# Performance work log

Measured on AMD Instinct MI355X. Metric: run time of the kernel, lower is better.

The kernel has to match this reference:

```python
import jax, jax.numpy as jnp
import numpy as np

N_DRUG, N_DIS, E, D = 10000, 15000, 1048576, 128

def setup_inputs() -> dict:
    key = jax.random.key(0)
    k = jax.random.split(key, 6)
    return {
        "z_drug": jax.random.normal(k[0], (N_DRUG, D), dtype=jnp.float32),
        "z_disease": jax.random.normal(k[1], (N_DIS, D), dtype=jnp.float32),
        "row": jax.random.randint(k[2], (E,), 0, N_DRUG),
        "col": jax.random.randint(k[3], (E,), 0, N_DIS),
        "W1": jax.random.normal(k[4], (2 * D, D), dtype=jnp.float32) * (1.0 / np.sqrt(2 * D)),
        "b1": jnp.zeros((D,), dtype=jnp.float32),
        "W2": jax.random.normal(k[5], (D, 1), dtype=jnp.float32) * (1.0 / np.sqrt(D)),
        "b2": jnp.zeros((1,), dtype=jnp.float32),
    }

def reference(z_drug, z_disease, row, col, W1, b1, W2, b2):
    # gather per-edge embeddings and concatenate: [E, 2D]
    z = jnp.concatenate([z_drug[row], z_disease[col]], axis=-1)
    h = jax.nn.relu(z @ W1 + b1)          # [E, D]
    out = h @ W2 + b2                      # [E, 1]
    return out.reshape(-1)                 # [E]
```

## Files before the change

kernel.cpp:

```cpp
#include <hip/hip_runtime.h>

typedef __attribute__((ext_vector_type(8))) short short8;
typedef __attribute__((ext_vector_type(4))) float floatx4;
typedef _Float16 half8 __attribute__((ext_vector_type(8)));
typedef _Float16 half4 __attribute__((ext_vector_type(4)));
typedef _Float16 half2v __attribute__((ext_vector_type(2)));

static __device__ __forceinline__ unsigned short f2bf(float x) {
    unsigned int u = __builtin_bit_cast(unsigned int, x);
    unsigned int r = (u + 0x7FFFu + ((u >> 16) & 1u)) >> 16;
    return (unsigned short)r;
}

__global__ void prep_w1(const float* __restrict__ W1, unsigned short* __restrict__ w1t) {
    int i = blockIdx.x * 256 + threadIdx.x;
    int n = i >> 8;
    int k = i & 255;
    w1t[n * 256 + k] = f2bf(W1[k * 128 + n]);
}

__global__ __launch_bounds__(256, 2) void factor_gemm(
    const float* __restrict__ zd, const float* __restrict__ zs,
    const unsigned short* __restrict__ w1t, const float* __restrict__ b1,
    _Float16* __restrict__ ud, _Float16* __restrict__ us,
    int ndrows, int nsrows, int ntd)
{
    const int tid  = threadIdx.x;
    const int lane = tid & 63;
    const int wave = tid >> 6;
    const int wh   = wave >> 1;
    const int we   = wave & 1;
    const int l15  = lane & 15;
    const int quad = lane >> 4;

    const int b = blockIdx.x;
    const bool isD = (b < ntd);
    const float* __restrict__ z = isD ? zd : zs;
    _Float16* __restrict__ u = isD ? ud : us;
    const int nrows = isD ? ndrows : nsrows;
    const int m0    = (isD ? b : b - ntd) * 64;
    const int koff0 = isD ? 0 : 128;

    short8 wfrag[16];
    #pragma unroll
    for (int s = 0; s < 4; ++s)
        #pragma unroll
        for (int mt = 0; mt < 4; ++mt)
            wfrag[s * 4 + mt] = *reinterpret_cast<const short8*>(
                &w1t[(size_t)(wh * 64 + mt * 16 + l15) * 256 + koff0 + s * 32 + quad * 8]);

    floatx4 acc[2][4];
    #pragma unroll
    for (int mt = 0; mt < 4; ++mt) {
        floatx4 bb = *reinterpret_cast<const floatx4*>(&b1[wh * 64 + mt * 16 + quad * 4]);
        bb *= 0.5f;
        acc[0][mt] = bb;
        acc[1][mt] = bb;
    }

    int rowi[2], rowc[2];
    #pragma unroll
    for (int et = 0; et < 2; ++et) {
        rowi[et] = m0 + we * 32 + et * 16 + l15;
        rowc[et] = rowi[et] < nrows ? rowi[et] : nrows - 1;
    }

    #pragma unroll
    for (int s = 0; s < 4; ++s) {
        short8 bf[2];
        #pragma unroll
        for (int et = 0; et < 2; ++et) {
            const float* src = &z[(size_t)rowc[et] * 128 + s * 32 + quad * 8];
            floatx4 lo = *reinterpret_cast<const floatx4*>(src);
            floatx4 hi = *reinterpret_cast<const floatx4*>(src + 4);
            short8 t;
            t[0] = (short)f2bf(lo[0]); t[1] = (short)f2bf(lo[1]);
            t[2] = (short)f2bf(lo[2]); t[3] = (short)f2bf(lo[3]);
            t[4] = (short)f2bf(hi[0]); t[5] = (short)f2bf(hi[1]);
            t[6] = (short)f2bf(hi[2]); t[7] = (short)f2bf(hi[3]);
            bf[et] = t;
        }
        #pragma unroll
        for (int et = 0; et < 2; ++et)
            #pragma unroll
            for (int mt = 0; mt < 4; ++mt)
                acc[et][mt] = __builtin_amdgcn_mfma_f32_16x16x32_bf16(
                    wfrag[s * 4 + mt], bf[et], acc[et][mt], 0, 0, 0);
    }

    #pragma unroll
    for (int et = 0; et < 2; ++et) {
        if (rowi[et] < nrows) {
            #pragma unroll
            for (int mt = 0; mt < 4; ++mt) {
                half4 hv;
                #pragma unroll
                for (int rr = 0; rr < 4; ++rr) hv[rr] = (_Float16)acc[et][mt][rr];
                *reinterpret_cast<half4*>(
                    &u[(size_t)rowi[et] * 128 + wh * 64 + mt * 16 + quad * 4]) = hv;
            }
        }
    }
}

__global__ __launch_bounds__(256, 4) void edge_eval(
    const _Float16* __restrict__ ud, const _Float16* __restrict__ us,
    const int* __restrict__ row, const int* __restrict__ col,
    const float* __restrict__ w2, const float* __restrict__ b2,
    float* __restrict__ out, int nchunks)
{
    const int tid  = threadIdx.x;
    const int lane = tid & 63;
    const int wave = tid >> 6;
    const int le   = lane >> 3;
    const int q    = lane & 7;
    const int lslot = wave * 8 + le;

#if __has_builtin(__builtin_amdgcn_fdot2)
    half2v w2h[8];
    #pragma unroll
    for (int i = 0; i < 2; ++i)
        #pragma unroll
        for (int p = 0; p < 4; ++p) {
            half2v t;
            t[0] = (_Float16)w2[i * 64 + q * 8 + 2 * p];
            t[1] = (_Float16)w2[i * 64 + q * 8 + 2 * p + 1];
            w2h[i * 4 + p] = t;
        }
#else
    float w2r[16];
    #pragma unroll
    for (int i = 0; i < 2; ++i) {
        *reinterpret_cast<floatx4*>(&w2r[i * 8]) =
            *reinterpret_cast<const floatx4*>(&w2[i * 64 + q * 8]);
        *reinterpret_cast<floatx4*>(&w2r[i * 8 + 4]) =
            *reinterpret_cast<const floatx4*>(&w2[i * 64 + q * 8 + 4]);
    }
#endif
    const float b2v = b2[0];
    const int G = gridDim.x;
    const int b = blockIdx.x;
    const int NC = nchunks / G;

    int ridx[4], cidx[4];
    half8 Ur[4][2], Vr[4][2];

#define LIDX(slot, j)                                                          \
    if ((j) < NC) {                                                            \
        int e = (b + (j) * G) * 32 + lslot;                                    \
        ridx[slot] = row[e]; cidx[slot] = col[e];                              \
    }

#define GATH(slot, j)                                                          \
    if ((j) < NC) {                                                            \
        const _Float16* up = ud + (size_t)ridx[slot] * 128 + q * 8;            \
        const _Float16* vp = us + (size_t)cidx[slot] * 128 + q * 8;            \
        Ur[slot][0] = *reinterpret_cast<const half8*>(up);                     \
        Ur[slot][1] = *reinterpret_cast<const half8*>(up + 64);                \
        Vr[slot][0] = *reinterpret_cast<const half8*>(vp);                     \
        Vr[slot][1] = *reinterpret_cast<const half8*>(vp + 64);                \
    }

#if __has_builtin(__builtin_amdgcn_fdot2)
#define DOT(slot, accv)                                                        \
    _Pragma("unroll")                                                          \
    for (int i = 0; i < 2; ++i) {                                              \
        half8 s8 = Ur[slot][i] + Vr[slot][i];                                  \
        s8 = __builtin_elementwise_max(s8, (half8)(_Float16)0.f);              \
        _Pragma("unroll")                                                      \
        for (int p = 0; p < 4; ++p) {                                          \
            half2v pr; pr[0] = s8[2 * p]; pr[1] = s8[2 * p + 1];               \
            accv = __builtin_amdgcn_fdot2(pr, w2h[i * 4 + p], accv, false);    \
        }                                                                      \
    }
#else
#define DOT(slot, accv)                                                        \
    _Pragma("unroll")                                                          \
    for (int i = 0; i < 2; ++i) {                                              \
        half8 s8 = Ur[slot][i] + Vr[slot][i];                                  \
        s8 = __builtin_elementwise_max(s8, (half8)(_Float16)0.f);              \
        _Pragma("unroll")                                                      \
        for (int j2 = 0; j2 < 8; ++j2)                                         \
            accv += (float)s8[j2] * w2r[i * 8 + j2];                           \
    }
#endif

#define COMP(slot, j)                                                          \
    if ((j) < NC) {                                                            \
        float acc = 0.f;                                                       \
        DOT(slot, acc)                                                         \
        acc += __shfl_xor(acc, 1);                                             \
        acc += __shfl_xor(acc, 2);                                             \
        acc += __shfl_xor(acc, 4);                                             \
        if (q == 0) out[(b + (j) * G) * 32 + lslot] = acc + b2v;               \
    }

    LIDX(0, 0) LIDX(1, 1) LIDX(2, 2)
    GATH(0, 0) GATH(1, 1) GATH(2, 2)
    LIDX(3, 3) LIDX(0, 4)

    for (int jb = 0; jb < NC; jb += 4) {
        GATH(3, jb + 3) LIDX(1, jb + 5) COMP(0, jb)
        GATH(0, jb + 4) LIDX(2, jb + 6) COMP(1, jb + 1)
        GATH(1, jb + 5) LIDX(3, jb + 7) COMP(2, jb + 2)
        GATH(2, jb + 6) LIDX(0, jb + 8) COMP(3, jb + 3)
    }
#undef LIDX
#undef GATH
#undef DOT
#undef COMP
}

extern "C" void kernel_launch(void* const* d_in, const int* in_sizes, int n_in,
                              void* d_out, int out_size, void* d_ws, size_t ws_size,
                              hipStream_t stream) {
    const float* zd = (const float*)d_in[0];
    const float* zs = (const float*)d_in[1];
    const int*   row = (const int*)d_in[2];
    const int*   col = (const int*)d_in[3];
    const float* W1 = (const float*)d_in[4];
    const float* b1 = (const float*)d_in[5];
    const float* w2 = (const float*)d_in[6];
    const float* b2 = (const float*)d_in[7];
    float* out = (float*)d_out;

    const int nd = in_sizes[0];
    const int ns = in_sizes[1];
    const int E  = in_sizes[2];
    const int ndrows = nd / 128;
    const int nsrows = ns / 128;

    unsigned short* w1t = (unsigned short*)d_ws;
    _Float16* ud = (_Float16*)((char*)d_ws + 128 * 256 * sizeof(unsigned short));
    _Float16* us = ud + (size_t)ndrows * 128;

    hipLaunchKernelGGL(prep_w1, dim3(128), dim3(256), 0, stream, W1, w1t);

    const int ntd = (ndrows + 63) / 64;
    const int nts = (nsrows + 63) / 64;
    hipLaunchKernelGGL(factor_gemm, dim3(ntd + nts), dim3(256), 0, stream,
                       zd, zs, w1t, b1, ud, us, ndrows, nsrows, ntd);

    const int nchunks = E / 32;
    const int egrid = 1024;
    hipLaunchKernelGGL(edge_eval, dim3(egrid), dim3(256), 0, stream,
                       ud, us, row, col, w2, b2, out, nchunks);
}
```

Before: 126.3 us.

## Bin edges by table half and map bins to XCDs for L2 locality

Adds a binning pass, fused into the factor GEMM launch, that splits edges into four classes by which half of the drug and disease tables they touch. Positions come from wave ballots and global atomics, and each class writes a packed row/col index plus the original edge id. The edge evaluation then assigns each class to a pair of XCDs (block index mod 8), so each XCD's L2 only holds a quarter of the factor tables. The cost is extra index traffic, an atomic-based compaction, scattered output writes, and an assumption that block-to-XCD assignment is round-robin.

```diff
diff --git a/kernel.cpp b/kernel.cpp
--- a/kernel.cpp
+++ b/kernel.cpp
@@ -12,102 +12,170 @@
     return (unsigned short)r;
 }
 
-__global__ void prep_w1(const float* __restrict__ W1, unsigned short* __restrict__ w1t) {
+__global__ void prep_w1(const float* __restrict__ W1, unsigned short* __restrict__ w1t,
+                        unsigned* __restrict__ gcur) {
     int i = blockIdx.x * 256 + threadIdx.x;
     int n = i >> 8;
     int k = i & 255;
     w1t[n * 256 + k] = f2bf(W1[k * 128 + n]);
-}
-
-__global__ __launch_bounds__(256, 2) void factor_gemm(
+    if (i < 16) gcur[i] = 0;
+}
+
+__global__ __launch_bounds__(256, 2) void mid_kernel(
     const float* __restrict__ zd, const float* __restrict__ zs,
     const unsigned short* __restrict__ w1t, const float* __restrict__ b1,
     _Float16* __restrict__ ud, _Float16* __restrict__ us,
-    int ndrows, int nsrows, int ntd)
+    int ndrows, int nsrows, int ntd, int nbg,
+    const int* __restrict__ row, const int* __restrict__ col,
+    unsigned* __restrict__ gcur, unsigned* __restrict__ rcbuf,
+    unsigned* __restrict__ eidbuf, int E)
 {
-    const int tid  = threadIdx.x;
-    const int lane = tid & 63;
-    const int wave = tid >> 6;
-    const int wh   = wave >> 1;
-    const int we   = wave & 1;
-    const int l15  = lane & 15;
-    const int quad = lane >> 4;
-
-    const int b = blockIdx.x;
-    const bool isD = (b < ntd);
-    const float* __restrict__ z = isD ? zd : zs;
-    _Float16* __restrict__ u = isD ? ud : us;
-    const int nrows = isD ? ndrows : nsrows;
-    const int m0    = (isD ? b : b - ntd) * 64;
-    const int koff0 = isD ? 0 : 128;
-
-    short8 wfrag[16];
-    #pragma unroll
-    for (int s = 0; s < 4; ++s)
-        #pragma unroll
-        for (int mt = 0; mt < 4; ++mt)
-            wfrag[s * 4 + mt] = *reinterpret_cast<const short8*>(
-                &w1t[(size_t)(wh * 64 + mt * 16 + l15) * 256 + koff0 + s * 32 + quad * 8]);
-
-    floatx4 acc[2][4];
-    #pragma unroll
-    for (int mt = 0; mt < 4; ++mt) {
-        floatx4 bb = *reinterpret_cast<const floatx4*>(&b1[wh * 64 + mt * 16 + quad * 4]);
-        bb *= 0.5f;
-        acc[0][mt] = bb;
-        acc[1][mt] = bb;
-    }
-
-    int rowi[2], rowc[2];
-    #pragma unroll
-    for (int et = 0; et < 2; ++et) {
-        rowi[et] = m0 + we * 32 + et * 16 + l15;
-        rowc[et] = rowi[et] < nrows ? rowi[et] : nrows - 1;
-    }
-
-    #pragma unroll
-    for (int s = 0; s < 4; ++s) {
-        short8 bf[2];
-        #pragma unroll
-        for (int et = 0; et < 2; ++et) {
-            const float* src = &z[(size_t)rowc[et] * 128 + s * 32 + quad * 8];
-            floatx4 lo = *reinterpret_cast<const floatx4*>(src);
-            floatx4 hi = *reinterpret_cast<const floatx4*>(src + 4);
-            short8 t;
-            t[0] = (short)f2bf(lo[0]); t[1] = (short)f2bf(lo[1]);
-            t[2] = (short)f2bf(lo[2]); t[3] = (short)f2bf(lo[3]);
-            t[4] = (short)f2bf(hi[0]); t[5] = (short)f2bf(hi[1]);
-            t[6] = (short)f2bf(hi[2]); t[7] = (short)f2bf(hi[3]);
-            bf[et] = t;
-        }
-        #pragma unroll
-        for (int et = 0; et < 2; ++et)
+    if ((int)blockIdx.x < nbg) {
+        const int tid  = threadIdx.x;
+        const int lane = tid & 63;
+        const int wave = tid >> 6;
+        const int wh   = wave >> 1;
+        const int we   = wave & 1;
+        const int l15  = lane & 15;
+        const int quad = lane >> 4;
+
+        const int b = blockIdx.x;
+        const bool isD = (b < ntd);
+        const float* __restrict__ z = isD ? zd : zs;
+        _Float16* __restrict__ u = isD ? ud : us;
+        const int nrows = isD ? ndrows : nsrows;
+        const int m0    = (isD ? b : b - ntd) * 64;
+        const int koff0 = isD ? 0 : 128;
+
+        short8 wfrag[16];
+        #pragma unroll
+        for (int s = 0; s < 4; ++s)
             #pragma unroll
             for (int mt = 0; mt < 4; ++mt)
-                acc[et][mt] = __builtin_amdgcn_mfma_f32_16x16x32_bf16(
-                    wfrag[s * 4 + mt], bf[et], acc[et][mt], 0, 0, 0);
+                wfrag[s * 4 + mt] = *reinterpret_cast<const short8*>(
+                    &w1t[(size_t)(wh * 64 + mt * 16 + l15) * 256 + koff0 + s * 32 + quad * 8]);
+
+        floatx4 acc[2][4];
+        #pragma unroll
+        for (int mt = 0; mt < 4; ++mt) {
+            floatx4 bb = *reinterpret_cast<const floatx4*>(&b1[wh * 64 + mt * 16 + quad * 4]);
+            bb *= 0.5f;
+            acc[0][mt] = bb;
+            acc[1][mt] = bb;
+        }
+
+        int rowi[2], rowc[2];
+        #pragma unroll
+        for (int et = 0; et < 2; ++et) {
+            rowi[et] = m0 + we * 32 + et * 16 + l15;
+            rowc[et] = rowi[et] < nrows ? rowi[et] : nrows - 1;
+        }
+
+        #pragma unroll
+        for (int s = 0; s < 4; ++s) {
+            short8 bf[2];
+            #pragma unroll
+            for (int et = 0; et < 2; ++et) {
+                const float* src = &z[(size_t)rowc[et] * 128 + s * 32 + quad * 8];
+                floatx4 lo = *reinterpret_cast<const floatx4*>(src);
+                floatx4 hi = *reinterpret_cast<const floatx4*>(src + 4);
+                short8 t;
+                t[0] = (short)f2bf(lo[0]); t[1] = (short)f2bf(lo[1]);
+                t[2] = (short)f2bf(lo[2]); t[3] = (short)f2bf(lo[3]);
+                t[4] = (short)f2bf(hi[0]); t[5] = (short)f2bf(hi[1]);
+                t[6] = (short)f2bf(hi[2]); t[7] = (short)f2bf(hi[3]);
+                bf[et] = t;
+            }
+            #pragma unroll
+            for (int et = 0; et < 2; ++et)
+                #pragma unroll
+                for (int mt = 0; mt < 4; ++mt)
+                    acc[et][mt] = __builtin_amdgcn_mfma_f32_16x16x32_bf16(
+                        wfrag[s * 4 + mt], bf[et], acc[et][mt], 0, 0, 0);
+        }
+
+        #pragma unroll
+        for (int et = 0; et < 2; ++et) {
+            if (rowi[et] < nrows) {
+                #pragma unroll
+                for (int mt = 0; mt < 4; ++mt) {
+                    half4 hv;
+                    #pragma unroll
+                    for (int rr = 0; rr < 4; ++rr) hv[rr] = (_Float16)acc[et][mt][rr];
+                    *reinterpret_cast<half4*>(
+                        &u[(size_t)rowi[et] * 128 + wh * 64 + mt * 16 + quad * 4]) = hv;
+                }
+            }
+        }
+    } else {
+        __shared__ unsigned wl[4][4];
+        __shared__ unsigned gb[4];
+        const int tid  = threadIdx.x;
+        const int lane = tid & 63;
+        const int wave = tid >> 6;
+        const int sb   = blockIdx.x - nbg;
+        const long base = (long)sb * 2048;
+
+        unsigned rc[8], off[8];
+        int cls0, cls1, cls2, cls3, cls4, cls5, cls6, cls7;
+        unsigned w0 = 0, w1 = 0, w2c = 0, w3 = 0;
+
+        #pragma unroll
+        for (int k = 0; k < 8; ++k) {
+            long e = base + wave * 512 + k * 64 + lane;
+            int r = row[e], c = col[e];
+            rc[k] = (unsigned)r | ((unsigned)c << 14);
+            int cl = ((r >= 5000) ? 2 : 0) | ((c >= 7500) ? 1 : 0);
+            unsigned long long m0 = __ballot(cl == 0);
+            unsigned long long m1 = __ballot(cl == 1);
+            unsigned long long m2 = __ballot(cl == 2);
+            unsigned long long m3 = __ballot(cl == 3);
+            unsigned long long mlt = (1ull << lane) - 1ull;
+            unsigned long long mc = (cl == 0) ? m0 : (cl == 1) ? m1 : (cl == 2) ? m2 : m3;
+            unsigned wb = (cl == 0) ? w0 : (cl == 1) ? w1 : (cl == 2) ? w2c : w3;
+            off[k] = wb + (unsigned)__popcll(mc & mlt);
+            w0 += (unsigned)__popcll(m0); w1 += (unsigned)__popcll(m1);
+            w2c += (unsigned)__popcll(m2); w3 += (unsigned)__popcll(m3);
+            switch (k) {
+                case 0: cls0 = cl; break; case 1: cls1 = cl; break;
+                case 2: cls2 = cl; break; case 3: cls3 = cl; break;
+                case 4: cls4 = cl; break; case 5: cls5 = cl; break;
+                case 6: cls6 = cl; break; default: cls7 = cl; break;
+            }
+        }
+        if (lane < 4) {
+            unsigned wv = (lane == 0) ? w0 : (lane == 1) ? w1 : (lane == 2) ? w2c : w3;
+            wl[wave][lane] = wv;
+        }
+        __syncthreads();
+        if (tid < 4) {
+            unsigned tot = wl[0][tid] + wl[1][tid] + wl[2][tid] + wl[3][tid];
+            gb[tid] = atomicAdd(&gcur[tid], tot);
+        }
+        __syncthreads();
+        unsigned p0 = 0, p1 = 0, p2 = 0, p3 = 0;
+        for (int w = 0; w < 4; ++w)
+            if (w < wave) { p0 += wl[w][0]; p1 += wl[w][1]; p2 += wl[w][2]; p3 += wl[w][3]; }
+
+        #pragma unroll
+        for (int k = 0; k < 8; ++k) {
+            long e = base + wave * 512 + k * 64 + lane;
+            int cl = (k == 0) ? cls0 : (k == 1) ? cls1 : (k == 2) ? cls2 : (k == 3) ? cls3
+                   : (k == 4) ? cls4 : (k == 5) ? cls5 : (k == 6) ? cls6 : cls7;
+            unsigned pre = (cl == 0) ? p0 : (cl == 1) ? p1 : (cl == 2) ? p2 : p3;
+            unsigned pos = gb[cl] + pre + off[k];
+            rcbuf[(size_t)cl * E + pos]  = rc[k];
+            eidbuf[(size_t)cl * E + pos] = (unsigned)e;
+        }
     }
-
-    #pragma unroll
-    for (int et = 0; et < 2; ++et) {
-        if (rowi[et] < nrows) {
-            #pragma unroll
-            for (int mt = 0; mt < 4; ++mt) {
-                half4 hv;
-                #pragma unroll
-                for (int rr = 0; rr < 4; ++rr) hv[rr] = (_Float16)acc[et][mt][rr];
-                *reinterpret_cast<half4*>(
-                    &u[(size_t)rowi[et] * 128 + wh * 64 + mt * 16 + quad * 4]) = hv;
-            }
-        }
-    }
-}
-
-__global__ __launch_bounds__(256, 4) void edge_eval(
+}
+
+__global__ __launch_bounds__(256, 8) void edge_eval(
     const _Float16* __restrict__ ud, const _Float16* __restrict__ us,
-    const int* __restrict__ row, const int* __restrict__ col,
+    const unsigned* __restrict__ gcur, const unsigned* __restrict__ rcbuf,
+    const unsigned* __restrict__ eidbuf,
     const float* __restrict__ w2, const float* __restrict__ b2,
-    float* __restrict__ out, int nchunks)
+    float* __restrict__ out, int E)
 {
     const int tid  = threadIdx.x;
     const int lane = tid & 63;
@@ -115,6 +183,17 @@
     const int le   = lane >> 3;
     const int q    = lane & 7;
     const int lslot = wave * 8 + le;
+
+    const int b    = blockIdx.x;
+    const int xcd  = b & 7;
+    const int cls  = xcd >> 1;
+    const int sub  = ((b >> 3) << 1) | (xcd & 1);
+    const int NSUB = (int)((gridDim.x >> 3) << 1);
+
+    const unsigned n = gcur[cls];
+    const int nch = (int)((n + 31u) >> 5);
+    const unsigned* __restrict__ rcb = rcbuf + (size_t)cls * E;
+    const unsigned* __restrict__ eib = eidbuf + (size_t)cls * E;
 
 #if __has_builtin(__builtin_amdgcn_fdot2)
     half2v w2h[8];
@@ -138,77 +217,65 @@
     }
 #endif
     const float b2v = b2[0];
-    const int G = gridDim.x;
-    const int b = blockIdx.x;
-    const int NC = nchunks / G;
-
-    int ridx[4], cidx[4];
-    half8 Ur[4][2], Vr[4][2];
-
-#define LIDX(slot, j)                                                          \
-    if ((j) < NC) {                                                            \
-        int e = (b + (j) * G) * 32 + lslot;                                    \
-        ridx[slot] = row[e]; cidx[slot] = col[e];                              \
+
+    int t = sub;
+    if (t >= nch) return;
+
+    unsigned ei0 = (unsigned)t * 32u + (unsigned)lslot;
+    bool v0 = ei0 < n;
+    unsigned ci0 = v0 ? ei0 : 0u;
+    unsigned rc0 = rcb[ci0];
+    unsigned id0 = eib[ci0];
+
+    while (true) {
+        const int tn = t + NSUB;
+
+        unsigned r = rc0 & 16383u, c = rc0 >> 14;
+        const _Float16* up = ud + (size_t)r * 128 + q * 8;
+        const _Float16* vp = us + (size_t)c * 128 + q * 8;
+        half8 U0 = *reinterpret_cast<const half8*>(up);
+        half8 U1 = *reinterpret_cast<const half8*>(up + 64);
+        half8 V0 = *reinterpret_cast<const half8*>(vp);
+        half8 V1 = *reinterpret_cast<const half8*>(vp + 64);
+
+        unsigned rc1 = 0, id1 = 0;
+        bool v1 = false;
+        if (tn < nch) {
+            unsigned ei1 = (unsigned)tn * 32u + (unsigned)lslot;
+            v1 = ei1 < n;
+            unsigned ci1 = v1 ? ei1 : 0u;
+            rc1 = rcb[ci1];
+            id1 = eib[ci1];
+        }
+
+        float acc = 0.f;
+        half8 s0 = U0 + V0;
+        s0 = __builtin_elementwise_max(s0, (half8)(_Float16)0.f);
+        half8 s1 = U1 + V1;
+        s1 = __builtin_elementwise_max(s1, (half8)(_Float16)0.f);
+#if __has_builtin(__builtin_amdgcn_fdot2)
+        #pragma unroll
+        for (int p = 0; p < 4; ++p) {
+            half2v pr0; pr0[0] = s0[2 * p]; pr0[1] = s0[2 * p + 1];
+            acc = __builtin_amdgcn_fdot2(pr0, w2h[p], acc, false);
+            half2v pr1; pr1[0] = s1[2 * p]; pr1[1] = s1[2 * p + 1];
+            acc = __builtin_amdgcn_fdot2(pr1, w2h[4 + p], acc, false);
+        }
+#else
+        #pragma unroll
+        for (int j = 0; j < 8; ++j) {
+            acc += (float)s0[j] * w2r[j];
+            acc += (float)s1[j] * w2r[8 + j];
+        }
+#endif
+        acc += __shfl_xor(acc, 1);
+        acc += __shfl_xor(acc, 2);
+        acc += __shfl_xor(acc, 4);
+        if (v0 && q == 0) out[id0] = acc + b2v;
+
+        if (tn >= nch) break;
+        t = tn; rc0 = rc1; id0 = id1; v0 = v1;
     }
-
-#define GATH(slot, j)                                                          \
-    if ((j) < NC) {                                                            \
-        const _Float16* up = ud + (size_t)ridx[slot] * 128 + q * 8;            \
-        const _Float16* vp = us + (size_t)cidx[slot] * 128 + q * 8;            \
-        Ur[slot][0] = *reinterpret_cast<const half8*>(up);                     \
-        Ur[slot][1] = *reinterpret_cast<const half8*>(up + 64);                \
-        Vr[slot][0] = *reinterpret_cast<const half8*>(vp);                     \
-        Vr[slot][1] = *reinterpret_cast<const half8*>(vp + 64);                \
-    }
-
-#if __has_builtin(__builtin_amdgcn_fdot2)
-#define DOT(slot, accv)                                                        \
-    _Pragma("unroll")                                                          \
-    for (int i = 0; i < 2; ++i) {                                              \
-        half8 s8 = Ur[slot][i] + Vr[slot][i];                                  \
-        s8 = __builtin_elementwise_max(s8, (half8)(_Float16)0.f);              \
-        _Pragma("unroll")                                                      \
-        for (int p = 0; p < 4; ++p) {                                          \
-            half2v pr; pr[0] = s8[2 * p]; pr[1] = s8[2 * p + 1];               \
-            accv = __builtin_amdgcn_fdot2(pr, w2h[i * 4 + p], accv, false);    \
-        }                                                                      \
-    }
-#else
-#define DOT(slot, accv)                                                        \
-    _Pragma("unroll")                                                          \
-    for (int i = 0; i < 2; ++i) {                                              \
-        half8 s8 = Ur[slot][i] + Vr[slot][i];                                  \
-        s8 = __builtin_elementwise_max(s8, (half8)(_Float16)0.f);              \
-        _Pragma("unroll")                                                      \
-        for (int j2 = 0; j2 < 8; ++j2)                                         \
-            accv += (float)s8[j2] * w2r[i * 8 + j2];                           \
-    }
-#endif
-
-#define COMP(slot, j)                                                          \
-    if ((j) < NC) {                                                            \
-        float acc = 0.f;                                                       \
-        DOT(slot, acc)                                                         \
-        acc += __shfl_xor(acc, 1);                                             \
-        acc += __shfl_xor(acc, 2);                                             \
-        acc += __shfl_xor(acc, 4);                                             \
-        if (q == 0) out[(b + (j) * G) * 32 + lslot] = acc + b2v;               \
-    }
-
-    LIDX(0, 0) LIDX(1, 1) LIDX(2, 2)
-    GATH(0, 0) GATH(1, 1) GATH(2, 2)
-    LIDX(3, 3) LIDX(0, 4)
-
-    for (int jb = 0; jb < NC; jb += 4) {
-        GATH(3, jb + 3) LIDX(1, jb + 5) COMP(0, jb)
-        GATH(0, jb + 4) LIDX(2, jb + 6) COMP(1, jb + 1)
-        GATH(1, jb + 5) LIDX(3, jb + 7) COMP(2, jb + 2)
-        GATH(2, jb + 6) LIDX(0, jb + 8) COMP(3, jb + 3)
-    }
-#undef LIDX
-#undef GATH
-#undef DOT
-#undef COMP
 }
 
 extern "C" void kernel_launch(void* const* d_in, const int* in_sizes, int n_in,
@@ -233,16 +300,22 @@
     unsigned short* w1t = (unsigned short*)d_ws;
     _Float16* ud = (_Float16*)((char*)d_ws + 128 * 256 * sizeof(unsigned short));
     _Float16* us = ud + (size_t)ndrows * 128;
-
-    hipLaunchKernelGGL(prep_w1, dim3(128), dim3(256), 0, stream, W1, w1t);
+    size_t off = (size_t)((char*)(us + (size_t)nsrows * 128) - (char*)d_ws);
+    off = (off + 63) & ~(size_t)63;
+    unsigned* gcur   = (unsigned*)((char*)d_ws + off);
+    unsigned* rcbuf  = gcur + 16;
+    unsigned* eidbuf = rcbuf + (size_t)4 * E;
+
+    hipLaunchKernelGGL(prep_w1, dim3(128), dim3(256), 0, stream, W1, w1t, gcur);
 
     const int ntd = (ndrows + 63) / 64;
     const int nts = (nsrows + 63) / 64;
-    hipLaunchKernelGGL(factor_gemm, dim3(ntd + nts), dim3(256), 0, stream,
-                       zd, zs, w1t, b1, ud, us, ndrows, nsrows, ntd);
-
-    const int nchunks = E / 32;
-    const int egrid = 1024;
-    hipLaunchKernelGGL(edge_eval, dim3(egrid), dim3(256), 0, stream,
-                       ud, us, row, col, w2, b2, out, nchunks);
-}
+    const int nbg = ntd + nts;
+    const int nsb = E / 2048;
+    hipLaunchKernelGGL(mid_kernel, dim3(nbg + nsb), dim3(256), 0, stream,
+                       zd, zs, w1t, b1, ud, us, ndrows, nsrows, ntd, nbg,
+                       row, col, gcur, rcbuf, eidbuf, E);
+
+    hipLaunchKernelGGL(edge_eval, dim3(2048), dim3(256), 0, stream,
+                       ud, us, gcur, rcbuf, eidbuf, w2, b2, out, E);
+}
```

Result: faster. 122.1 us (-3.3%).
